# Kernel tuning notes

Hardware: AMD Instinct MI355X
Metric: run time of the kernel (lower is better)

## Reference

```python
import jax, jax.numpy as jnp
import numpy as np

PATCH_LEN = 16


def _forward(x, W_proj, b_proj, W_router, b_router, W_experts, b_experts, W_head, b_head):
    # x: (B, L, C); Model drops first 2 channels
    seq_len = x.shape[1]
    xs = x[:, :, 2:]                                   # (B, L, N)
    B, L, N = xs.shape
    # CI=True: 'b l n -> (b n) l 1' (track as (BN, L) since trailing dim is 1)
    ci = jnp.transpose(xs, (0, 2, 1)).reshape(B * N, L)
    # RevIN-style instance norm (means detached in torch)
    means = jax.lax.stop_gradient(jnp.mean(ci, axis=1, keepdims=True))
    xc = ci - means
    stdev = jnp.sqrt(jnp.var(xc, axis=1, keepdims=True) + 1e-5)  # unbiased=False
    xc = xc / stdev
    # non-overlapping patching: unfold(1, pl, pl)
    p = L // PATCH_LEN
    patches = xc[:, : p * PATCH_LEN].reshape(B * N, p, PATCH_LEN)
    xp = patches @ W_proj.T + b_proj                   # (BN, p, d)
    gates = jax.nn.softmax(xp @ W_router.T + b_router, axis=-1)  # (BN, p, E)
    # soft-routed mixture of linear experts: sum_e gate_e * (xp @ W_e^T + b_e)
    eo = jnp.einsum('tpd,ehd->tpeh', xp, W_experts) + b_experts  # (BN, p, E, d)
    combined = jnp.einsum('tpeh,tpe->tph', eo, gates)            # (BN, p, d)
    d = combined.shape[-1]
    flat = combined.reshape(B * N, p * d)              # '(b n) p d -> b (p d) n', n=1
    if p * d < seq_len:
        flat = jnp.pad(flat, ((0, 0), (0, seq_len - p * d)))
    else:
        flat = flat[:, :seq_len]
    flat = flat * stdev + means                        # de-normalize (BN, L)
    # '(b n) l 1 -> b l n' then 'b l n -> b n l' == reshape to (B, N, L)
    temporal = flat.reshape(B, N, seq_len)
    out = temporal @ W_head.T + b_head                 # linear_head: (B, N, pred)
    out = jnp.transpose(out, (0, 2, 1))[:, :, :1]      # 'b n d -> b d n', keep var 0
    return out


def setup_inputs() -> dict:
    key = jax.random.key(0)
    ks = jax.random.split(key, 12)
    B, L, C = 32, 1024, 34
    d, E, pl, pred = 256, 8, PATCH_LEN, 96
    return {
        'x': jax.random.normal(ks[0], (B, L, C), dtype=jnp.float32),
        'x_mark_enc': jax.random.normal(ks[1], (B, L, 4), dtype=jnp.float32),
        'x_dec': jax.random.normal(ks[2], (B, pred, C), dtype=jnp.float32),
        'x_mark_dec': jax.random.normal(ks[3], (B, pred, 4), dtype=jnp.float32),
        'W_proj': jax.random.normal(ks[4], (d, pl), dtype=jnp.float32) * 0.1,
        'b_proj': jax.random.normal(ks[5], (d,), dtype=jnp.float32) * 0.02,
        'W_router': jax.random.normal(ks[6], (E, d), dtype=jnp.float32) * 0.05,
        'b_router': jax.random.normal(ks[7], (E,), dtype=jnp.float32) * 0.02,
        'W_experts': jax.random.normal(ks[8], (E, d, d), dtype=jnp.float32) * 0.05,
        'b_experts': jax.random.normal(ks[9], (E, d), dtype=jnp.float32) * 0.02,
        'W_head': jax.random.normal(ks[10], (pred, L), dtype=jnp.float32) * 0.03,
        'b_head': jax.random.normal(ks[11], (pred,), dtype=jnp.float32) * 0.02,
    }


def reference(x, x_mark_enc, x_dec, x_mark_dec, W_proj, b_proj, W_router, b_router,
              W_experts, b_experts, W_head, b_head):
    # x_mark_enc, x_dec, x_mark_dec are accepted but unused by Model.forward
    return _forward(x, W_proj, b_proj, W_router, b_router,
                    W_experts, b_experts, W_head, b_head)
```

## Files before the change

kernel.cpp:

```cpp
#include <hip/hip_runtime.h>
#include <math.h>


#define NB 32
#define LSEQ 1024
#define CCH 34
#define NP 4
#define DMODEL 256
#define NEXP 8
#define PRED 96
#define DT 64
#define NPART NEXP

#define STATS_FLOATS (NB * 2)

__global__ __launch_bounds__(256) void k_fused(
    const float* __restrict__ x,
    const float* __restrict__ W_proj, const float* __restrict__ b_proj,
    const float* __restrict__ W_router, const float* __restrict__ b_router,
    const float* __restrict__ W_experts, const float* __restrict__ b_experts,
    float* __restrict__ flat_part, float* __restrict__ stats_ws)
{
    const int bid = blockIdx.x;
    const int e   = bid & 7;
    const int b   = bid >> 3;
    const int tid = threadIdx.x;

    __shared__ float wtT[DT][DMODEL + 1];
    __shared__ float xn[LSEQ];
    __shared__ float xp_s[NP * DMODEL];
    __shared__ float red[8];
    __shared__ float lg[32];
    __shared__ float g_s[NP];
    __shared__ float mean_s, rstd_s;

    float v[4];
    #pragma unroll
    for (int i = 0; i < 4; ++i)
        v[i] = x[(size_t)(b * LSEQ + tid + 256 * i) * CCH + 2];

    const int c4 = tid & 15;
    const int hb = tid >> 4;
    const float* wsrc = W_experts + ((size_t)e << 16);
    float4 wreg[16];
    #pragma unroll
    for (int i = 0; i < 16; ++i)
        wreg[i] = *(const float4*)(wsrc + (size_t)(hb + 16 * i) * DMODEL + 4 * c4);

    {
        float s = 0.f, sq = 0.f;
        #pragma unroll
        for (int i = 0; i < 4; ++i) { s += v[i]; sq += v[i] * v[i]; }
        #pragma unroll
        for (int off = 32; off > 0; off >>= 1) {
            s  += __shfl_down(s,  off);
            sq += __shfl_down(sq, off);
        }
        const int wave = tid >> 6;
        if ((tid & 63) == 0) { red[wave * 2] = s; red[wave * 2 + 1] = sq; }
        __syncthreads();
        if (tid == 0) {
            const float S = red[0] + red[2] + red[4] + red[6];
            const float Q = red[1] + red[3] + red[5] + red[7];
            const float mean = S * (1.0f / LSEQ);
            const float var  = Q * (1.0f / LSEQ) - mean * mean;
            const float stdv = sqrtf(var + 1e-5f);
            mean_s = mean;
            rstd_s = 1.0f / stdv;
            if (e == 0) {
                stats_ws[b * 2]     = mean;
                stats_ws[b * 2 + 1] = stdv;
            }
        }
        __syncthreads();
        const float mean = mean_s, rstd = rstd_s;
        #pragma unroll
        for (int i = 0; i < 4; ++i)
            xn[tid + 256 * i] = (v[i] - mean) * rstd;
        __syncthreads();
    }

    {
        const int h = tid;
        float wrow[16];
        #pragma unroll
        for (int j = 0; j < 16; ++j) wrow[j] = W_proj[h * 16 + j];
        const float bp = b_proj[h];
        #pragma unroll
        for (int p = 0; p < NP; ++p) {
            float acc = bp;
            #pragma unroll
            for (int j = 0; j < 16; ++j) acc += xn[p * 16 + j] * wrow[j];
            xp_s[p * DMODEL + h] = acc;
        }
    }
    __syncthreads();

    {
        const int pe = tid >> 3;
        const int sl = tid & 7;
        const int p  = pe >> 3;
        const int er = pe & 7;
        float acc = 0.f;
        #pragma unroll 8
        for (int j = 0; j < 32; ++j) {
            const int hh = sl + 8 * j;
            acc += xp_s[p * DMODEL + hh] * W_router[er * DMODEL + hh];
        }
        acc += __shfl_xor(acc, 4);
        acc += __shfl_xor(acc, 2);
        acc += __shfl_xor(acc, 1);
        if (sl == 0) lg[pe] = acc + b_router[er];
    }
    __syncthreads();

    if (tid < NP) {
        const int p = tid;
        float m = -1e30f;
        #pragma unroll
        for (int k = 0; k < NEXP; ++k) m = fmaxf(m, lg[p * 8 + k]);
        float ex[NEXP];
        float sum = 0.f;
        #pragma unroll
        for (int k = 0; k < NEXP; ++k) { ex[k] = expf(lg[p * 8 + k] - m); sum += ex[k]; }
        g_s[p] = ex[e] / sum;
    }

    float acc0 = 0.f, acc1 = 0.f, acc2 = 0.f, acc3 = 0.f;
    for (int t = 0; t < 4; ++t) {
        __syncthreads();
        #pragma unroll
        for (int i = 0; i < 16; ++i) {
            const int h = hb + 16 * i;
            wtT[4 * c4 + 0][h] = wreg[i].x;
            wtT[4 * c4 + 1][h] = wreg[i].y;
            wtT[4 * c4 + 2][h] = wreg[i].z;
            wtT[4 * c4 + 3][h] = wreg[i].w;
        }
        __syncthreads();
        if (t < 3) {
            #pragma unroll
            for (int i = 0; i < 16; ++i)
                wreg[i] = *(const float4*)(wsrc + (size_t)(hb + 16 * i) * DMODEL
                                           + (t + 1) * DT + 4 * c4);
        }
        const float* xpp = xp_s + t * DT;
        #pragma unroll 8
        for (int c = 0; c < DT; ++c) {
            const float wv = wtT[c][tid];
            acc0 += xpp[c]       * wv;
            acc1 += xpp[256 + c] * wv;
            acc2 += xpp[512 + c] * wv;
            acc3 += xpp[768 + c] * wv;
        }
    }

    const float bias = b_experts[(e << 8) + tid];
    const size_t base = ((size_t)(e * NB + b) << 10) + tid;
    flat_part[base]         = g_s[0] * (acc0 + bias);
    flat_part[base + 256]   = g_s[1] * (acc1 + bias);
    flat_part[base + 512]   = g_s[2] * (acc2 + bias);
    flat_part[base + 768]   = g_s[3] * (acc3 + bias);
}

__global__ __launch_bounds__(256) void k_head(
    const float* __restrict__ flat_part, const float* __restrict__ stats_ws,
    const float* __restrict__ W_head, const float* __restrict__ b_head,
    float* __restrict__ out)
{
    const int b   = blockIdx.x >> 3;
    const int kq  = blockIdx.x & 7;
    const int tid = threadIdx.x;
    __shared__ float4 f4s[DMODEL];

    const float mean = stats_ws[b * 2];
    const float stdv = stats_ws[b * 2 + 1];

    {
        float4 acc = make_float4(0.f, 0.f, 0.f, 0.f);
        #pragma unroll
        for (int i = 0; i < NPART; ++i) {
            const float4 t = ((const float4*)(flat_part + (((size_t)i * NB + b) << 10)))[tid];
            acc.x += t.x; acc.y += t.y; acc.z += t.z; acc.w += t.w;
        }
        acc.x = acc.x * stdv + mean;
        acc.y = acc.y * stdv + mean;
        acc.z = acc.z * stdv + mean;
        acc.w = acc.w * stdv + mean;
        f4s[tid] = acc;
    }
    __syncthreads();

    const int lane = tid & 63;
    const int w    = tid >> 6;
    float4 fr[4];
    #pragma unroll
    for (int c = 0; c < 4; ++c) fr[c] = f4s[lane + 64 * c];

    #pragma unroll
    for (int i = 0; i < 3; ++i) {
        const int k = kq * 12 + w + 4 * i;
        const float4* wr = (const float4*)(W_head + (size_t)k * LSEQ);
        float a = 0.f;
        #pragma unroll
        for (int c = 0; c < 4; ++c) {
            const float4 t = wr[lane + 64 * c];
            a += t.x * fr[c].x + t.y * fr[c].y + t.z * fr[c].z + t.w * fr[c].w;
        }
        #pragma unroll
        for (int off = 32; off > 0; off >>= 1)
            a += __shfl_xor(a, off);
        if (lane == 0)
            out[(size_t)b * PRED + k] = b_head[k] + a;
    }
}

extern "C" void kernel_launch(void* const* d_in, const int* in_sizes, int n_in,
                              void* d_out, int out_size, void* d_ws, size_t ws_size,
                              hipStream_t stream)
{
    const float* x         = (const float*)d_in[0];
    const float* W_proj    = (const float*)d_in[4];
    const float* b_proj    = (const float*)d_in[5];
    const float* W_router  = (const float*)d_in[6];
    const float* b_router  = (const float*)d_in[7];
    const float* W_experts = (const float*)d_in[8];
    const float* b_experts = (const float*)d_in[9];
    const float* W_head    = (const float*)d_in[10];
    const float* b_head    = (const float*)d_in[11];
    float* out = (float*)d_out;
    float* ws  = (float*)d_ws;

    float* stats_ws  = ws;
    float* flat_part = ws + STATS_FLOATS;

    k_fused<<<256, 256, 0, stream>>>(x, W_proj, b_proj, W_router, b_router,
                                     W_experts, b_experts, flat_part, stats_ws);
    k_head<<<256, 256, 0, stream>>>(flat_part, stats_ws, W_head, b_head, out);
}
```

Baseline: 98.83 us.

## Merge expert and head kernels into one cooperative launch with grid sync

```diff
diff --git a/kernel.cpp b/kernel.cpp
--- a/kernel.cpp
+++ b/kernel.cpp
@@ -1,5 +1,8 @@
 #include <hip/hip_runtime.h>
+#include <hip/hip_cooperative_groups.h>
 #include <math.h>
+
+namespace cg = cooperative_groups;
 
 
 #define NB 32
@@ -14,204 +17,214 @@
 
 #define STATS_FLOATS (NB * 2)
 
-__global__ __launch_bounds__(256) void k_fused(
+#define PH_BOTH   0
+#define PH_EXPERT 1
+#define PH_HEAD   2
+
+__global__ __launch_bounds__(256) void k_all(
     const float* __restrict__ x,
     const float* __restrict__ W_proj, const float* __restrict__ b_proj,
     const float* __restrict__ W_router, const float* __restrict__ b_router,
     const float* __restrict__ W_experts, const float* __restrict__ b_experts,
-    float* __restrict__ flat_part, float* __restrict__ stats_ws)
+    const float* __restrict__ W_head, const float* __restrict__ b_head,
+    float* __restrict__ flat_part, float* __restrict__ stats_ws,
+    float* __restrict__ out, int phase)
 {
     const int bid = blockIdx.x;
-    const int e   = bid & 7;
-    const int b   = bid >> 3;
     const int tid = threadIdx.x;
 
     __shared__ float wtT[DT][DMODEL + 1];
-    __shared__ float xn[LSEQ];
+    __shared__ __align__(16) float xn[LSEQ];
     __shared__ float xp_s[NP * DMODEL];
     __shared__ float red[8];
     __shared__ float lg[32];
     __shared__ float g_s[NP];
     __shared__ float mean_s, rstd_s;
 
-    float v[4];
-    #pragma unroll
-    for (int i = 0; i < 4; ++i)
-        v[i] = x[(size_t)(b * LSEQ + tid + 256 * i) * CCH + 2];
-
-    const int c4 = tid & 15;
-    const int hb = tid >> 4;
-    const float* wsrc = W_experts + ((size_t)e << 16);
-    float4 wreg[16];
-    #pragma unroll
-    for (int i = 0; i < 16; ++i)
-        wreg[i] = *(const float4*)(wsrc + (size_t)(hb + 16 * i) * DMODEL + 4 * c4);
-
-    {
-        float s = 0.f, sq = 0.f;
-        #pragma unroll
-        for (int i = 0; i < 4; ++i) { s += v[i]; sq += v[i] * v[i]; }
-        #pragma unroll
-        for (int off = 32; off > 0; off >>= 1) {
-            s  += __shfl_down(s,  off);
-            sq += __shfl_down(sq, off);
-        }
-        const int wave = tid >> 6;
-        if ((tid & 63) == 0) { red[wave * 2] = s; red[wave * 2 + 1] = sq; }
+    if (phase != PH_HEAD) {
+        const int e = bid & 7;
+        const int b = bid >> 3;
+
+        float v[4];
+        #pragma unroll
+        for (int i = 0; i < 4; ++i)
+            v[i] = x[(size_t)(b * LSEQ + tid + 256 * i) * CCH + 2];
+
+        const int c4 = tid & 15;
+        const int hb = tid >> 4;
+        const float* wsrc = W_experts + ((size_t)e << 16);
+        float4 wreg[16];
+        #pragma unroll
+        for (int i = 0; i < 16; ++i)
+            wreg[i] = *(const float4*)(wsrc + (size_t)(hb + 16 * i) * DMODEL + 4 * c4);
+
+        {
+            float s = 0.f, sq = 0.f;
+            #pragma unroll
+            for (int i = 0; i < 4; ++i) { s += v[i]; sq += v[i] * v[i]; }
+            #pragma unroll
+            for (int off = 32; off > 0; off >>= 1) {
+                s  += __shfl_down(s,  off);
+                sq += __shfl_down(sq, off);
+            }
+            const int wave = tid >> 6;
+            if ((tid & 63) == 0) { red[wave * 2] = s; red[wave * 2 + 1] = sq; }
+            __syncthreads();
+            if (tid == 0) {
+                const float S = red[0] + red[2] + red[4] + red[6];
+                const float Q = red[1] + red[3] + red[5] + red[7];
+                const float mean = S * (1.0f / LSEQ);
+                const float var  = Q * (1.0f / LSEQ) - mean * mean;
+                const float stdv = sqrtf(var + 1e-5f);
+                mean_s = mean;
+                rstd_s = 1.0f / stdv;
+                if (e == 0) {
+                    stats_ws[b * 2]     = mean;
+                    stats_ws[b * 2 + 1] = stdv;
+                }
+            }
+            __syncthreads();
+            const float mean = mean_s, rstd = rstd_s;
+            #pragma unroll
+            for (int i = 0; i < 4; ++i)
+                xn[tid + 256 * i] = (v[i] - mean) * rstd;
+            __syncthreads();
+        }
+
+        {
+            const int h = tid;
+            float wrow[16];
+            #pragma unroll
+            for (int j = 0; j < 16; ++j) wrow[j] = W_proj[h * 16 + j];
+            const float bp = b_proj[h];
+            #pragma unroll
+            for (int p = 0; p < NP; ++p) {
+                float acc = bp;
+                #pragma unroll
+                for (int j = 0; j < 16; ++j) acc += xn[p * 16 + j] * wrow[j];
+                xp_s[p * DMODEL + h] = acc;
+            }
+        }
         __syncthreads();
-        if (tid == 0) {
-            const float S = red[0] + red[2] + red[4] + red[6];
-            const float Q = red[1] + red[3] + red[5] + red[7];
-            const float mean = S * (1.0f / LSEQ);
-            const float var  = Q * (1.0f / LSEQ) - mean * mean;
-            const float stdv = sqrtf(var + 1e-5f);
-            mean_s = mean;
-            rstd_s = 1.0f / stdv;
-            if (e == 0) {
-                stats_ws[b * 2]     = mean;
-                stats_ws[b * 2 + 1] = stdv;
-            }
+
+        {
+            const int pe = tid >> 3;
+            const int sl = tid & 7;
+            const int p  = pe >> 3;
+            const int er = pe & 7;
+            float acc = 0.f;
+            #pragma unroll 8
+            for (int j = 0; j < 32; ++j) {
+                const int hh = sl + 8 * j;
+                acc += xp_s[p * DMODEL + hh] * W_router[er * DMODEL + hh];
+            }
+            acc += __shfl_xor(acc, 4);
+            acc += __shfl_xor(acc, 2);
+            acc += __shfl_xor(acc, 1);
+            if (sl == 0) lg[pe] = acc + b_router[er];
         }
         __syncthreads();
-        const float mean = mean_s, rstd = rstd_s;
-        #pragma unroll
-        for (int i = 0; i < 4; ++i)
-            xn[tid + 256 * i] = (v[i] - mean) * rstd;
+
+        if (tid < NP) {
+            const int p = tid;
+            float m = -1e30f;
+            #pragma unroll
+            for (int k = 0; k < NEXP; ++k) m = fmaxf(m, lg[p * 8 + k]);
+            float ex[NEXP];
+            float sum = 0.f;
+            #pragma unroll
+            for (int k = 0; k < NEXP; ++k) { ex[k] = expf(lg[p * 8 + k] - m); sum += ex[k]; }
+            g_s[p] = ex[e] / sum;
+        }
+
+        float acc0 = 0.f, acc1 = 0.f, acc2 = 0.f, acc3 = 0.f;
+        for (int t = 0; t < 4; ++t) {
+            __syncthreads();
+            #pragma unroll
+            for (int i = 0; i < 16; ++i) {
+                const int h = hb + 16 * i;
+                wtT[4 * c4 + 0][h] = wreg[i].x;
+                wtT[4 * c4 + 1][h] = wreg[i].y;
+                wtT[4 * c4 + 2][h] = wreg[i].z;
+                wtT[4 * c4 + 3][h] = wreg[i].w;
+            }
+            __syncthreads();
+            if (t < 3) {
+                #pragma unroll
+                for (int i = 0; i < 16; ++i)
+                    wreg[i] = *(const float4*)(wsrc + (size_t)(hb + 16 * i) * DMODEL
+                                               + (t + 1) * DT + 4 * c4);
+            }
+            const float* xpp = xp_s + t * DT;
+            #pragma unroll 8
+            for (int c = 0; c < DT; ++c) {
+                const float wv = wtT[c][tid];
+                acc0 += xpp[c]       * wv;
+                acc1 += xpp[256 + c] * wv;
+                acc2 += xpp[512 + c] * wv;
+                acc3 += xpp[768 + c] * wv;
+            }
+        }
+
+        const float bias = b_experts[(e << 8) + tid];
+        const size_t base = ((size_t)(e * NB + b) << 10) + tid;
+        flat_part[base]         = g_s[0] * (acc0 + bias);
+        flat_part[base + 256]   = g_s[1] * (acc1 + bias);
+        flat_part[base + 512]   = g_s[2] * (acc2 + bias);
+        flat_part[base + 768]   = g_s[3] * (acc3 + bias);
+    }
+
+    if (phase == PH_BOTH) {
+        __threadfence();
+        cg::this_grid().sync();
+    }
+
+    if (phase != PH_EXPERT) {
+        const int b  = bid >> 3;
+        const int kq = bid & 7;
+        float4* f4s = (float4*)xn;
+
+        const float mean = stats_ws[b * 2];
+        const float stdv = stats_ws[b * 2 + 1];
+
+        {
+            float4 acc = make_float4(0.f, 0.f, 0.f, 0.f);
+            #pragma unroll
+            for (int i = 0; i < NPART; ++i) {
+                const float4 t =
+                    ((const float4*)(flat_part + (((size_t)i * NB + b) << 10)))[tid];
+                acc.x += t.x; acc.y += t.y; acc.z += t.z; acc.w += t.w;
+            }
+            acc.x = acc.x * stdv + mean;
+            acc.y = acc.y * stdv + mean;
+            acc.z = acc.z * stdv + mean;
+            acc.w = acc.w * stdv + mean;
+            f4s[tid] = acc;
+        }
         __syncthreads();
-    }
-
-    {
-        const int h = tid;
-        float wrow[16];
-        #pragma unroll
-        for (int j = 0; j < 16; ++j) wrow[j] = W_proj[h * 16 + j];
-        const float bp = b_proj[h];
-        #pragma unroll
-        for (int p = 0; p < NP; ++p) {
-            float acc = bp;
-            #pragma unroll
-            for (int j = 0; j < 16; ++j) acc += xn[p * 16 + j] * wrow[j];
-            xp_s[p * DMODEL + h] = acc;
-        }
-    }
-    __syncthreads();
-
-    {
-        const int pe = tid >> 3;
-        const int sl = tid & 7;
-        const int p  = pe >> 3;
-        const int er = pe & 7;
-        float acc = 0.f;
-        #pragma unroll 8
-        for (int j = 0; j < 32; ++j) {
-            const int hh = sl + 8 * j;
-            acc += xp_s[p * DMODEL + hh] * W_router[er * DMODEL + hh];
-        }
-        acc += __shfl_xor(acc, 4);
-        acc += __shfl_xor(acc, 2);
-        acc += __shfl_xor(acc, 1);
-        if (sl == 0) lg[pe] = acc + b_router[er];
-    }
-    __syncthreads();
-
-    if (tid < NP) {
-        const int p = tid;
-        float m = -1e30f;
-        #pragma unroll
-        for (int k = 0; k < NEXP; ++k) m = fmaxf(m, lg[p * 8 + k]);
-        float ex[NEXP];
-        float sum = 0.f;
-        #pragma unroll
-        for (int k = 0; k < NEXP; ++k) { ex[k] = expf(lg[p * 8 + k] - m); sum += ex[k]; }
-        g_s[p] = ex[e] / sum;
-    }
-
-    float acc0 = 0.f, acc1 = 0.f, acc2 = 0.f, acc3 = 0.f;
-    for (int t = 0; t < 4; ++t) {
-        __syncthreads();
-        #pragma unroll
-        for (int i = 0; i < 16; ++i) {
-            const int h = hb + 16 * i;
-            wtT[4 * c4 + 0][h] = wreg[i].x;
-            wtT[4 * c4 + 1][h] = wreg[i].y;
-            wtT[4 * c4 + 2][h] = wreg[i].z;
-            wtT[4 * c4 + 3][h] = wreg[i].w;
-        }
-        __syncthreads();
-        if (t < 3) {
-            #pragma unroll
-            for (int i = 0; i < 16; ++i)
-                wreg[i] = *(const float4*)(wsrc + (size_t)(hb + 16 * i) * DMODEL
-                                           + (t + 1) * DT + 4 * c4);
-        }
-        const float* xpp = xp_s + t * DT;
-        #pragma unroll 8
-        for (int c = 0; c < DT; ++c) {
-            const float wv = wtT[c][tid];
-            acc0 += xpp[c]       * wv;
-            acc1 += xpp[256 + c] * wv;
-            acc2 += xpp[512 + c] * wv;
-            acc3 += xpp[768 + c] * wv;
-        }
-    }
-
-    const float bias = b_experts[(e << 8) + tid];
-    const size_t base = ((size_t)(e * NB + b) << 10) + tid;
-    flat_part[base]         = g_s[0] * (acc0 + bias);
-    flat_part[base + 256]   = g_s[1] * (acc1 + bias);
-    flat_part[base + 512]   = g_s[2] * (acc2 + bias);
-    flat_part[base + 768]   = g_s[3] * (acc3 + bias);
-}
-
-__global__ __launch_bounds__(256) void k_head(
-    const float* __restrict__ flat_part, const float* __restrict__ stats_ws,
-    const float* __restrict__ W_head, const float* __restrict__ b_head,
-    float* __restrict__ out)
-{
-    const int b   = blockIdx.x >> 3;
-    const int kq  = blockIdx.x & 7;
-    const int tid = threadIdx.x;
-    __shared__ float4 f4s[DMODEL];
-
-    const float mean = stats_ws[b * 2];
-    const float stdv = stats_ws[b * 2 + 1];
-
-    {
-        float4 acc = make_float4(0.f, 0.f, 0.f, 0.f);
-        #pragma unroll
-        for (int i = 0; i < NPART; ++i) {
-            const float4 t = ((const float4*)(flat_part + (((size_t)i * NB + b) << 10)))[tid];
-            acc.x += t.x; acc.y += t.y; acc.z += t.z; acc.w += t.w;
-        }
-        acc.x = acc.x * stdv + mean;
-        acc.y = acc.y * stdv + mean;
-        acc.z = acc.z * stdv + mean;
-        acc.w = acc.w * stdv + mean;
-        f4s[tid] = acc;
-    }
-    __syncthreads();
-
-    const int lane = tid & 63;
-    const int w    = tid >> 6;
-    float4 fr[4];
-    #pragma unroll
-    for (int c = 0; c < 4; ++c) fr[c] = f4s[lane + 64 * c];
-
-    #pragma unroll
-    for (int i = 0; i < 3; ++i) {
-        const int k = kq * 12 + w + 4 * i;
-        const float4* wr = (const float4*)(W_head + (size_t)k * LSEQ);
-        float a = 0.f;
-        #pragma unroll
-        for (int c = 0; c < 4; ++c) {
-            const float4 t = wr[lane + 64 * c];
-            a += t.x * fr[c].x + t.y * fr[c].y + t.z * fr[c].z + t.w * fr[c].w;
-        }
-        #pragma unroll
-        for (int off = 32; off > 0; off >>= 1)
-            a += __shfl_xor(a, off);
-        if (lane == 0)
-            out[(size_t)b * PRED + k] = b_head[k] + a;
+
+        const int lane = tid & 63;
+        const int w    = tid >> 6;
+        float4 fr[4];
+        #pragma unroll
+        for (int c = 0; c < 4; ++c) fr[c] = f4s[lane + 64 * c];
+
+        #pragma unroll
+        for (int i = 0; i < 3; ++i) {
+            const int k = kq * 12 + w + 4 * i;
+            const float4* wr = (const float4*)(W_head + (size_t)k * LSEQ);
+            float a = 0.f;
+            #pragma unroll
+            for (int c = 0; c < 4; ++c) {
+                const float4 t = wr[lane + 64 * c];
+                a += t.x * fr[c].x + t.y * fr[c].y + t.z * fr[c].z + t.w * fr[c].w;
+            }
+            #pragma unroll
+            for (int off = 32; off > 0; off >>= 1)
+                a += __shfl_xor(a, off);
+            if (lane == 0)
+                out[(size_t)b * PRED + k] = b_head[k] + a;
+        }
     }
 }
 
@@ -234,7 +247,24 @@
     float* stats_ws  = ws;
     float* flat_part = ws + STATS_FLOATS;
 
-    k_fused<<<256, 256, 0, stream>>>(x, W_proj, b_proj, W_router, b_router,
-                                     W_experts, b_experts, flat_part, stats_ws);
-    k_head<<<256, 256, 0, stream>>>(flat_part, stats_ws, W_head, b_head, out);
+    int phase = PH_BOTH;
+    void* args[] = {
+        (void*)&x, (void*)&W_proj, (void*)&b_proj, (void*)&W_router,
+        (void*)&b_router, (void*)&W_experts, (void*)&b_experts,
+        (void*)&W_head, (void*)&b_head, (void*)&flat_part,
+        (void*)&stats_ws, (void*)&out, (void*)&phase
+    };
+
+    hipError_t err = hipLaunchCooperativeKernel(
+        (const void*)k_all, dim3(256), dim3(256), args, 0, stream);
+
+    if (err != hipSuccess) {
+        (void)hipGetLastError();
+        k_all<<<256, 256, 0, stream>>>(x, W_proj, b_proj, W_router, b_router,
+                                       W_experts, b_experts, W_head, b_head,
+                                       flat_part, stats_ws, out, PH_EXPERT);
+        k_all<<<256, 256, 0, stream>>>(x, W_proj, b_proj, W_router, b_router,
+                                       W_experts, b_experts, W_head, b_head,
+                                       flat_part, stats_ws, out, PH_HEAD);
+    }
 }
```

Result: slower. 159.5 us (+61.4%).

## Use 1024-thread blocks with coalesced x loads and row-major expert tile

Applied to the files above, without the earlier changes.

```diff
diff --git a/kernel.cpp b/kernel.cpp
--- a/kernel.cpp
+++ b/kernel.cpp
@@ -13,8 +13,9 @@
 #define NPART NEXP
 
 #define STATS_FLOATS (NB * 2)
-
-__global__ __launch_bounds__(256) void k_fused(
+#define XCHUNKS ((LSEQ * CCH) / 4)
+
+__global__ __launch_bounds__(1024) void k_fused(
     const float* __restrict__ x,
     const float* __restrict__ W_proj, const float* __restrict__ b_proj,
     const float* __restrict__ W_router, const float* __restrict__ b_router,
@@ -22,35 +23,50 @@
     float* __restrict__ flat_part, float* __restrict__ stats_ws)
 {
     const int bid = blockIdx.x;
-    const int e   = bid & 7;
-    const int b   = bid >> 3;
+    const int e   = bid >> 5;
+    const int b   = bid & 31;
     const int tid = threadIdx.x;
 
-    __shared__ float wtT[DT][DMODEL + 1];
-    __shared__ float xn[LSEQ];
-    __shared__ float xp_s[NP * DMODEL];
-    __shared__ float red[8];
+    __shared__ __align__(16) float wtS[DMODEL][DT + 4];
+    __shared__ __align__(16) float xn[LSEQ];
+    __shared__ __align__(16) float xp_s[NP * DMODEL];
+    __shared__ float red[32];
     __shared__ float lg[32];
     __shared__ float g_s[NP];
     __shared__ float mean_s, rstd_s;
 
-    float v[4];
-    #pragma unroll
-    for (int i = 0; i < 4; ++i)
-        v[i] = x[(size_t)(b * LSEQ + tid + 256 * i) * CCH + 2];
+    {
+        const float4* xr = (const float4*)(x + (size_t)b * (LSEQ * CCH));
+        #pragma unroll
+        for (int j = 0; j < 9; ++j) {
+            const int k = tid + (j << 10);
+            if (k < XCHUNKS) {
+                const float4 f = xr[k];
+                const int base = 4 * k;
+                const int l0   = (base + 31) / 34;
+                const int off  = 34 * l0 + 2 - base;
+                if (off < 4 && l0 < LSEQ) {
+                    const float val = (off == 0) ? f.x : (off == 1) ? f.y
+                                    : (off == 2) ? f.z : f.w;
+                    xn[l0] = val;
+                }
+            }
+        }
+    }
 
     const int c4 = tid & 15;
     const int hb = tid >> 4;
     const float* wsrc = W_experts + ((size_t)e << 16);
-    float4 wreg[16];
+    float4 wreg[4];
     #pragma unroll
-    for (int i = 0; i < 16; ++i)
-        wreg[i] = *(const float4*)(wsrc + (size_t)(hb + 16 * i) * DMODEL + 4 * c4);
-
-    {
-        float s = 0.f, sq = 0.f;
-        #pragma unroll
-        for (int i = 0; i < 4; ++i) { s += v[i]; sq += v[i] * v[i]; }
+    for (int i = 0; i < 4; ++i)
+        wreg[i] = *(const float4*)(wsrc + (size_t)(hb + 64 * i) * DMODEL + 4 * c4);
+
+    __syncthreads();
+
+    {
+        const float v = xn[tid];
+        float s = v, sq = v * v;
         #pragma unroll
         for (int off = 32; off > 0; off >>= 1) {
             s  += __shfl_down(s,  off);
@@ -60,8 +76,9 @@
         if ((tid & 63) == 0) { red[wave * 2] = s; red[wave * 2 + 1] = sq; }
         __syncthreads();
         if (tid == 0) {
-            const float S = red[0] + red[2] + red[4] + red[6];
-            const float Q = red[1] + red[3] + red[5] + red[7];
+            float S = 0.f, Q = 0.f;
+            #pragma unroll
+            for (int w = 0; w < 16; ++w) { S += red[2 * w]; Q += red[2 * w + 1]; }
             const float mean = S * (1.0f / LSEQ);
             const float var  = Q * (1.0f / LSEQ) - mean * mean;
             const float stdv = sqrtf(var + 1e-5f);
@@ -73,39 +90,32 @@
             }
         }
         __syncthreads();
-        const float mean = mean_s, rstd = rstd_s;
-        #pragma unroll
-        for (int i = 0; i < 4; ++i)
-            xn[tid + 256 * i] = (v[i] - mean) * rstd;
-        __syncthreads();
-    }
-
-    {
-        const int h = tid;
-        float wrow[16];
-        #pragma unroll
-        for (int j = 0; j < 16; ++j) wrow[j] = W_proj[h * 16 + j];
-        const float bp = b_proj[h];
-        #pragma unroll
-        for (int p = 0; p < NP; ++p) {
-            float acc = bp;
-            #pragma unroll
-            for (int j = 0; j < 16; ++j) acc += xn[p * 16 + j] * wrow[j];
-            xp_s[p * DMODEL + h] = acc;
-        }
-    }
-    __syncthreads();
-
-    {
+        xn[tid] = (v - mean_s) * rstd_s;
+        __syncthreads();
+    }
+
+    const int p = tid >> 8;
+    const int h = tid & 255;
+
+    {
+        const float* wp = W_proj + h * 16;
+        float acc = b_proj[h];
+        #pragma unroll
+        for (int j = 0; j < 16; ++j) acc += xn[p * 16 + j] * wp[j];
+        xp_s[p * DMODEL + h] = acc;
+    }
+    __syncthreads();
+
+    if (tid < 256) {
         const int pe = tid >> 3;
         const int sl = tid & 7;
-        const int p  = pe >> 3;
+        const int pp = pe >> 3;
         const int er = pe & 7;
         float acc = 0.f;
         #pragma unroll 8
         for (int j = 0; j < 32; ++j) {
             const int hh = sl + 8 * j;
-            acc += xp_s[p * DMODEL + hh] * W_router[er * DMODEL + hh];
+            acc += xp_s[pp * DMODEL + hh] * W_router[er * DMODEL + hh];
         }
         acc += __shfl_xor(acc, 4);
         acc += __shfl_xor(acc, 2);
@@ -115,52 +125,42 @@
     __syncthreads();
 
     if (tid < NP) {
-        const int p = tid;
+        const int pp = tid;
         float m = -1e30f;
         #pragma unroll
-        for (int k = 0; k < NEXP; ++k) m = fmaxf(m, lg[p * 8 + k]);
+        for (int k = 0; k < NEXP; ++k) m = fmaxf(m, lg[pp * 8 + k]);
         float ex[NEXP];
         float sum = 0.f;
         #pragma unroll
-        for (int k = 0; k < NEXP; ++k) { ex[k] = expf(lg[p * 8 + k] - m); sum += ex[k]; }
-        g_s[p] = ex[e] / sum;
-    }
-
-    float acc0 = 0.f, acc1 = 0.f, acc2 = 0.f, acc3 = 0.f;
+        for (int k = 0; k < NEXP; ++k) { ex[k] = expf(lg[pp * 8 + k] - m); sum += ex[k]; }
+        g_s[pp] = ex[e] / sum;
+    }
+
+    float acc = 0.f;
     for (int t = 0; t < 4; ++t) {
         __syncthreads();
         #pragma unroll
-        for (int i = 0; i < 16; ++i) {
-            const int h = hb + 16 * i;
-            wtT[4 * c4 + 0][h] = wreg[i].x;
-            wtT[4 * c4 + 1][h] = wreg[i].y;
-            wtT[4 * c4 + 2][h] = wreg[i].z;
-            wtT[4 * c4 + 3][h] = wreg[i].w;
-        }
+        for (int i = 0; i < 4; ++i)
+            ((float4*)&wtS[hb + 64 * i][0])[c4] = wreg[i];
         __syncthreads();
         if (t < 3) {
             #pragma unroll
-            for (int i = 0; i < 16; ++i)
-                wreg[i] = *(const float4*)(wsrc + (size_t)(hb + 16 * i) * DMODEL
+            for (int i = 0; i < 4; ++i)
+                wreg[i] = *(const float4*)(wsrc + (size_t)(hb + 64 * i) * DMODEL
                                            + (t + 1) * DT + 4 * c4);
         }
-        const float* xpp = xp_s + t * DT;
-        #pragma unroll 8
-        for (int c = 0; c < DT; ++c) {
-            const float wv = wtT[c][tid];
-            acc0 += xpp[c]       * wv;
-            acc1 += xpp[256 + c] * wv;
-            acc2 += xpp[512 + c] * wv;
-            acc3 += xpp[768 + c] * wv;
-        }
-    }
-
-    const float bias = b_experts[(e << 8) + tid];
-    const size_t base = ((size_t)(e * NB + b) << 10) + tid;
-    flat_part[base]         = g_s[0] * (acc0 + bias);
-    flat_part[base + 256]   = g_s[1] * (acc1 + bias);
-    flat_part[base + 512]   = g_s[2] * (acc2 + bias);
-    flat_part[base + 768]   = g_s[3] * (acc3 + bias);
+        const float4* wrow = (const float4*)&wtS[h][0];
+        const float4* xpp  = (const float4*)&xp_s[p * DMODEL + t * DT];
+        #pragma unroll
+        for (int q = 0; q < 16; ++q) {
+            const float4 wv = wrow[q];
+            const float4 xv = xpp[q];
+            acc += wv.x * xv.x + wv.y * xv.y + wv.z * xv.z + wv.w * xv.w;
+        }
+    }
+
+    const float bias = b_experts[(e << 8) + h];
+    flat_part[(((size_t)(e * NB + b)) << 10) + (p << 8) + h] = g_s[p] * (acc + bias);
 }
 
 __global__ __launch_bounds__(256) void k_head(
@@ -180,7 +180,8 @@
         float4 acc = make_float4(0.f, 0.f, 0.f, 0.f);
         #pragma unroll
         for (int i = 0; i < NPART; ++i) {
-            const float4 t = ((const float4*)(flat_part + (((size_t)i * NB + b) << 10)))[tid];
+            const float4 t =
+                ((const float4*)(flat_part + (((size_t)i * NB + b) << 10)))[tid];
             acc.x += t.x; acc.y += t.y; acc.z += t.z; acc.w += t.w;
         }
         acc.x = acc.x * stdv + mean;
@@ -234,7 +235,7 @@
     float* stats_ws  = ws;
     float* flat_part = ws + STATS_FLOATS;
 
-    k_fused<<<256, 256, 0, stream>>>(x, W_proj, b_proj, W_router, b_router,
-                                     W_experts, b_experts, flat_part, stats_ws);
+    k_fused<<<256, 1024, 0, stream>>>(x, W_proj, b_proj, W_router, b_router,
+                                      W_experts, b_experts, flat_part, stats_ws);
     k_head<<<256, 256, 0, stream>>>(flat_part, stats_ws, W_head, b_head, out);
 }
```

Result: slower. 113.9 us (+15.3%).

## Split expert reduction dimension across two blocks and remap block indices

Applied to the files above, without the earlier changes.

```diff
diff --git a/kernel.cpp b/kernel.cpp
--- a/kernel.cpp
+++ b/kernel.cpp
@@ -10,11 +10,11 @@
 #define NEXP 8
 #define PRED 96
 #define DT 64
-#define NPART NEXP
+#define NPART (2 * NEXP)
 
 #define STATS_FLOATS (NB * 2)
 
-__global__ __launch_bounds__(256) void k_fused(
+__global__ __launch_bounds__(256, 2) void k_fused(
     const float* __restrict__ x,
     const float* __restrict__ W_proj, const float* __restrict__ b_proj,
     const float* __restrict__ W_router, const float* __restrict__ b_router,
@@ -22,9 +22,14 @@
     float* __restrict__ flat_part, float* __restrict__ stats_ws)
 {
     const int bid = blockIdx.x;
-    const int e   = bid & 7;
-    const int b   = bid >> 3;
-    const int tid = threadIdx.x;
+    const int lo   = bid & 7;
+    const int hi   = bid >> 3;
+    const int dh   = hi & 1;
+    const int t2   = hi >> 1;
+    const int b    = ((t2 & 7) << 2) | (lo >> 1);
+    const int e    = ((t2 >> 3) << 1) | (lo & 1);
+    const int tid  = threadIdx.x;
+    const int t0   = 2 * dh;
 
     __shared__ float wtT[DT][DMODEL + 1];
     __shared__ float xn[LSEQ];
@@ -45,7 +50,8 @@
     float4 wreg[16];
     #pragma unroll
     for (int i = 0; i < 16; ++i)
-        wreg[i] = *(const float4*)(wsrc + (size_t)(hb + 16 * i) * DMODEL + 4 * c4);
+        wreg[i] = *(const float4*)(wsrc + (size_t)(hb + 16 * i) * DMODEL
+                                   + t0 * DT + 4 * c4);
 
     {
         float s = 0.f, sq = 0.f;
@@ -67,7 +73,7 @@
             const float stdv = sqrtf(var + 1e-5f);
             mean_s = mean;
             rstd_s = 1.0f / stdv;
-            if (e == 0) {
+            if (e == 0 && dh == 0) {
                 stats_ws[b * 2]     = mean;
                 stats_ws[b * 2 + 1] = stdv;
             }
@@ -127,7 +133,7 @@
     }
 
     float acc0 = 0.f, acc1 = 0.f, acc2 = 0.f, acc3 = 0.f;
-    for (int t = 0; t < 4; ++t) {
+    for (int it = 0; it < 2; ++it) {
         __syncthreads();
         #pragma unroll
         for (int i = 0; i < 16; ++i) {
@@ -138,13 +144,13 @@
             wtT[4 * c4 + 3][h] = wreg[i].w;
         }
         __syncthreads();
-        if (t < 3) {
+        if (it == 0) {
             #pragma unroll
             for (int i = 0; i < 16; ++i)
                 wreg[i] = *(const float4*)(wsrc + (size_t)(hb + 16 * i) * DMODEL
-                                           + (t + 1) * DT + 4 * c4);
-        }
-        const float* xpp = xp_s + t * DT;
+                                           + (t0 + 1) * DT + 4 * c4);
+        }
+        const float* xpp = xp_s + (t0 + it) * DT;
         #pragma unroll 8
         for (int c = 0; c < DT; ++c) {
             const float wv = wtT[c][tid];
@@ -155,8 +161,9 @@
         }
     }
 
-    const float bias = b_experts[(e << 8) + tid];
-    const size_t base = ((size_t)(e * NB + b) << 10) + tid;
+    const float bias = (dh == 0) ? b_experts[(e << 8) + tid] : 0.f;
+    const int part = (e << 1) | dh;
+    const size_t base = ((size_t)(part * NB + b) << 10) + tid;
     flat_part[base]         = g_s[0] * (acc0 + bias);
     flat_part[base + 256]   = g_s[1] * (acc1 + bias);
     flat_part[base + 512]   = g_s[2] * (acc2 + bias);
@@ -180,7 +187,8 @@
         float4 acc = make_float4(0.f, 0.f, 0.f, 0.f);
         #pragma unroll
         for (int i = 0; i < NPART; ++i) {
-            const float4 t = ((const float4*)(flat_part + (((size_t)i * NB + b) << 10)))[tid];
+            const float4 t =
+                ((const float4*)(flat_part + (((size_t)i * NB + b) << 10)))[tid];
             acc.x += t.x; acc.y += t.y; acc.z += t.z; acc.w += t.w;
         }
         acc.x = acc.x * stdv + mean;
@@ -234,7 +242,7 @@
     float* stats_ws  = ws;
     float* flat_part = ws + STATS_FLOATS;
 
-    k_fused<<<256, 256, 0, stream>>>(x, W_proj, b_proj, W_router, b_router,
+    k_fused<<<512, 256, 0, stream>>>(x, W_proj, b_proj, W_router, b_router,
                                      W_experts, b_experts, flat_part, stats_ws);
     k_head<<<256, 256, 0, stream>>>(flat_part, stats_ws, W_head, b_head, out);
 }
```

New measurement: 96.61 us. 2.3% less time.
